# Kernel optimization log

Hardware: AMD Instinct MI355X
Metric: run time of the kernel (lower is better)

The kernel has to match this reference:

```python
import jax, jax.numpy as jnp
import numpy as np

B, N, E, D, H, C, U = 512, 256, 1024, 256, 256, 8, 64
MARGIN_T, RISK_T, SCALE = 0.2, 0.6, 0.1
NEG = -1.0e9


def setup_inputs() -> dict:
    key = jax.random.key(0)
    ks = jax.random.split(key, 30)
    s = 0.02
    inp = dict(
        features=jax.random.normal(ks[0], (B, D), jnp.float32),
        centered_scores=jax.random.normal(ks[1], (B, N), jnp.float32),
        margin=jax.random.uniform(ks[2], (B,), jnp.float32),
        boundary_risk=jax.random.uniform(ks[3], (B,), jnp.float32),
        edge_sensitivity=jax.random.normal(ks[4], (B, E), jnp.float32),
        coords=jax.random.normal(ks[5], (B, N, C), jnp.float32),
        uncertainty=jax.random.uniform(ks[6], (B, U), jnp.float32),
        Wc1=jax.random.normal(ks[7], (D, H), jnp.float32) * s,
        bc1=jnp.zeros((H,), jnp.float32),
        Wc2=jax.random.normal(ks[8], (H, H), jnp.float32) * s,
        bc2=jnp.zeros((H,), jnp.float32),
        Wn1=jax.random.normal(ks[9], (H + C + 2, H), jnp.float32) * s,
        bn1=jnp.zeros((H,), jnp.float32),
        Wn2=jax.random.normal(ks[10], (H, 1), jnp.float32) * s,
        bn2=jnp.zeros((1,), jnp.float32),
        We1=jax.random.normal(ks[11], (H + C + 2, H), jnp.float32) * s,
        be1=jnp.zeros((H,), jnp.float32),
        We2=jax.random.normal(ks[12], (H, 1), jnp.float32) * s,
        be2=jnp.zeros((1,), jnp.float32),
        Wg=jax.random.normal(ks[13], (H, 1), jnp.float32) * s,
        bg=jnp.zeros((1,), jnp.float32),
        action_mask=jax.random.bernoulli(ks[14], 0.8, (B, N)),
        edge_mask=jax.random.bernoulli(ks[15], 0.8, (B, E)),
        actions=jax.random.randint(ks[16], (B, N), 0, U, jnp.int32),
        edges=jax.random.randint(ks[17], (B, E, 2), 0, N, jnp.int32),
    )
    return inp


def _mlp2(x, W1, b1, W2, b2):
    return jax.nn.relu(x @ W1 + b1) @ W2 + b2


def reference(features, centered_scores, margin, boundary_risk, edge_sensitivity,
              coords, uncertainty, Wc1, bc1, Wc2, bc2, Wn1, bn1, Wn2, bn2,
              We1, be1, We2, be2, Wg, bg, action_mask, edge_mask, actions, edges):
    amf = action_mask.astype(jnp.float32)
    emf = edge_mask.astype(jnp.float32)

    # context MLP
    h = jax.nn.relu(jax.nn.relu(features @ Wc1 + bc1) @ Wc2 + bc2)  # [B,H]

    low_margin = (margin < MARGIN_T).astype(jnp.float32)
    high_risk = (boundary_risk > RISK_T).astype(jnp.float32)
    learned_gate = jax.nn.sigmoid((h @ Wg + bg)[:, 0])
    refine_gate = jnp.maximum(jnp.maximum(low_margin, high_risk),
                              (learned_gate > 0.5).astype(jnp.float32))  # [B]

    # node features: [B,N,H+C+2]
    act = jnp.clip(actions, 0, U - 1)
    unc_g = jnp.take_along_axis(uncertainty, act, axis=1)  # [B,N]
    h_n = jnp.broadcast_to(h[:, None, :], (B, N, H))
    node_feats = jnp.concatenate(
        [h_n, coords, centered_scores[..., None], unc_g[..., None]], axis=-1)
    node_delta = _mlp2(node_feats, Wn1, bn1, Wn2, bn2)[..., 0] * amf  # [B,N]

    # edge features: gather src/dst coords
    e = jnp.clip(edges, 0, N - 1)
    src_c = jnp.take_along_axis(coords, e[:, :, 0:1], axis=1)  # [B,E,C]
    dst_c = jnp.take_along_axis(coords, e[:, :, 1:2], axis=1)  # [B,E,C]
    h_e = jnp.broadcast_to(h[:, None, :], (B, E, H))
    edge_feats = jnp.concatenate(
        [h_e, dst_c - src_c, edge_sensitivity[..., None], emf[..., None]], axis=-1)
    edge_delta = _mlp2(edge_feats, We1, be1, We2, be2)[..., 0] * emf  # [B,E]

    gate_node = refine_gate[:, None]
    refined_scores = (centered_scores + gate_node * SCALE * node_delta) * amf
    denom = jnp.clip(amf.sum(-1, keepdims=True), 1.0, None)  # [B,1]
    refined_scores = (refined_scores - refined_scores.sum(-1, keepdims=True) / denom) * amf

    refined_edge = (edge_sensitivity + gate_node * SCALE * edge_delta) * emf

    masked_top = jnp.where(action_mask, refined_scores, NEG)
    top_vals, top_idx = jax.lax.top_k(masked_top, 2)
    refined_margin = top_vals[:, 0] - top_vals[:, 1]

    # masked per-batch variance of refined_edge (biased), 0 if <=1 valid entry
    cnt = emf.sum(-1)
    cnt_c = jnp.clip(cnt, 1.0, None)
    mean = (refined_edge * emf).sum(-1) / cnt_c
    var = (emf * (refined_edge - mean[:, None]) ** 2).sum(-1) / cnt_c
    edge_var = jnp.where(cnt > 1.0, var, 0.0)

    unc_term = (unc_g * amf).sum(-1) / denom[:, 0]
    refined_risk = jnp.clip(
        jax.nn.sigmoid(-refined_margin) + 0.2 * edge_var + 0.1 * unc_term, 0.0, 1.0)

    return (refined_scores, refined_margin, refined_edge,
            top_idx[:, 0], refined_risk, refine_gate)
```

## Files before the change

kernel.cpp:

```cpp
#include <hip/hip_runtime.h>
#include <math.h>

#define B 512
#define N 256
#define E 1024
#define D 256
#define H 256
#define C 8
#define U 64

typedef __fp16 h2 __attribute__((ext_vector_type(2)));
union UF { float f; h2 h; unsigned u; };

__device__ __forceinline__ float bc_f(h2 h) { UF u; u.h = h; return u.f; }
__device__ __forceinline__ h2 bc_h(float f) { UF u; u.f = f; return u.h; }

#if __has_builtin(__builtin_amdgcn_cvt_pkrtz)
__device__ __forceinline__ h2 pkh(float a, float b) { return __builtin_amdgcn_cvt_pkrtz(a, b); }
#else
__device__ __forceinline__ h2 pkh(float a, float b) { h2 r; r.x = (__fp16)a; r.y = (__fp16)b; return r; }
#endif

#if __has_builtin(__builtin_amdgcn_fdot2)
__device__ __forceinline__ float FDOT2(h2 a, h2 b, float c) { return __builtin_amdgcn_fdot2(a, b, c, false); }
#else
__device__ __forceinline__ float FDOT2(h2 a, h2 b, float c) {
    return fmaf((float)a.x, (float)b.x, fmaf((float)a.y, (float)b.y, c));
}
#endif

__device__ __forceinline__ float mask_val(const void* m, long i, int flag) {
    if (flag == 1) return ((const unsigned char*)m)[i] ? 1.f : 0.f;
    if (flag == 2) return (((const float*)m)[i] != 0.f) ? 1.f : 0.f;
    return ((const int*)m)[i] ? 1.f : 0.f;
}

__device__ __forceinline__ float block_sum(float v, float* red) {
    int t = threadIdx.x;
    red[t] = v; __syncthreads();
    for (int s = 128; s > 0; s >>= 1) {
        if (t < s) red[t] += red[t + s];
        __syncthreads();
    }
    float r = red[0]; __syncthreads();
    return r;
}

__global__ __launch_bounds__(512) void k_h(
    const float* __restrict__ feat,
    const float* __restrict__ Wc1, const float* __restrict__ bc1,
    const float* __restrict__ Wc2, const float* __restrict__ bc2,
    const float* __restrict__ Wn1, const float* __restrict__ bn1,
    const float* __restrict__ We1, const float* __restrict__ be1,
    const float* __restrict__ Wg,  const float* __restrict__ bg,
    const float* __restrict__ margin, const float* __restrict__ brisk,
    const unsigned int* __restrict__ amask_words,
    float* __restrict__ base_n, float* __restrict__ base_e,
    float* __restrict__ out_gate, int* __restrict__ flag)
{
    __shared__ __align__(16) float sF[4][256];
    __shared__ __align__(16) float sH[4][256];
    __shared__ float red[512];
    __shared__ int cls0, cls1;

    int t = threadIdx.x;
    int w = t >> 8;
    int c = t & 255;
    int b0 = blockIdx.x * 4;
    int r0 = 2 * w, r1 = 2 * w + 1;

    if (blockIdx.x == 0) {
        if (t == 0) { cls0 = 0; cls1 = 0; }
        __syncthreads();
        if (t < 256) {
            unsigned int wd = amask_words[t];
            if (wd != 0u && wd != 1u) {
                if (wd == 0x3f800000u) atomicOr(&cls1, 1);
                else                   atomicOr(&cls0, 1);
            }
        }
        __syncthreads();
        if (t == 0) *flag = cls0 ? 1 : (cls1 ? 2 : 0);
    }

    sF[r0][c] = feat[(long)(b0 + r0) * D + c];
    sF[r1][c] = feat[(long)(b0 + r1) * D + c];
    __syncthreads();

    {
        float aA[2] = {bc1[c], 0.f}, aB[2] = {bc1[c], 0.f};
        const float* Wp = Wc1 + c;
        for (int d0 = 0; d0 < D; d0 += 16) {
            float wv[16];
            #pragma unroll
            for (int k = 0; k < 16; k++) wv[k] = Wp[(long)(d0 + k) * H];
            #pragma unroll
            for (int k = 0; k < 16; k++) {
                aA[k & 1] = fmaf(sF[r0][d0 + k], wv[k], aA[k & 1]);
                aB[k & 1] = fmaf(sF[r1][d0 + k], wv[k], aB[k & 1]);
            }
        }
        sH[r0][c] = fmaxf(aA[0] + aA[1], 0.f);
        sH[r1][c] = fmaxf(aB[0] + aB[1], 0.f);
    }
    __syncthreads();

    {
        float aA[2] = {bc2[c], 0.f}, aB[2] = {bc2[c], 0.f};
        const float* Wp = Wc2 + c;
        for (int d0 = 0; d0 < H; d0 += 16) {
            float wv[16];
            #pragma unroll
            for (int k = 0; k < 16; k++) wv[k] = Wp[(long)(d0 + k) * H];
            #pragma unroll
            for (int k = 0; k < 16; k++) {
                aA[k & 1] = fmaf(sH[r0][d0 + k], wv[k], aA[k & 1]);
                aB[k & 1] = fmaf(sH[r1][d0 + k], wv[k], aB[k & 1]);
            }
        }
        float hA = fmaxf(aA[0] + aA[1], 0.f);
        float hB = fmaxf(aB[0] + aB[1], 0.f);
        __syncthreads();
        sF[r0][c] = hA;
        sF[r1][c] = hB;
    }
    __syncthreads();

    #pragma unroll
    for (int rr = 0; rr < 2; rr++) {
        int r = 2 * w + rr;
        red[t] = sF[r][c] * Wg[c];
        __syncthreads();
        for (int s = 128; s > 0; s >>= 1) {
            if (c < s) red[t] += red[t + s];
            __syncthreads();
        }
        if (c == 0) {
            int b = b0 + r;
            float lg = 1.f / (1.f + expf(-(red[t] + bg[0])));
            out_gate[b] = ((margin[b] < 0.2f) || (brisk[b] > 0.6f) || (lg > 0.5f)) ? 1.f : 0.f;
        }
        __syncthreads();
    }

    {
        const float* W3  = w ? (We1 + c) : (Wn1 + c);
        float bias       = w ? be1[c]    : bn1[c];
        float* dst       = w ? base_e    : base_n;
        float aA[2] = {bias, 0.f}, aB[2] = {bias, 0.f};
        float aC[2] = {bias, 0.f}, aD[2] = {bias, 0.f};
        for (int d0 = 0; d0 < H; d0 += 16) {
            float wv[16];
            #pragma unroll
            for (int k = 0; k < 16; k++) wv[k] = W3[(long)(d0 + k) * H];
            #pragma unroll
            for (int k = 0; k < 16; k++) {
                aA[k & 1] = fmaf(sF[0][d0 + k], wv[k], aA[k & 1]);
                aB[k & 1] = fmaf(sF[1][d0 + k], wv[k], aB[k & 1]);
                aC[k & 1] = fmaf(sF[2][d0 + k], wv[k], aC[k & 1]);
                aD[k & 1] = fmaf(sF[3][d0 + k], wv[k], aD[k & 1]);
            }
        }
        dst[(long)(b0 + 0) * H + c] = aA[0] + aA[1];
        dst[(long)(b0 + 1) * H + c] = aB[0] + aB[1];
        dst[(long)(b0 + 2) * H + c] = aC[0] + aC[1];
        dst[(long)(b0 + 3) * H + c] = aD[0] + aD[1];
    }
}

__global__ __launch_bounds__(256, 2) void k_ne(
    const float* __restrict__ cs, const float* __restrict__ coords,
    const float* __restrict__ unc, const int* __restrict__ actions,
    const void* __restrict__ amask,
    const float* __restrict__ Wn1, const float* __restrict__ Wn2,
    const float* __restrict__ bn2, const float* __restrict__ base_n,
    const float* __restrict__ es, const int* __restrict__ edges,
    const void* __restrict__ emask,
    const float* __restrict__ We1, const float* __restrict__ We2,
    const float* __restrict__ be2, const float* __restrict__ base_e,
    const float* __restrict__ gate, const int* __restrict__ flagp,
    float* __restrict__ out0, float* __restrict__ out1,
    float* __restrict__ out2, float* __restrict__ out3,
    float* __restrict__ riskbase, float* __restrict__ evar)
{
    __shared__ __align__(16) float smem[4864];
    int t = threadIdx.x;
    int w = t >> 6, lane = t & 63;
    int flag = *flagp;

    if (blockIdx.x < 128) {
        float* pack = smem;
        float* sB   = smem + 3072;
        int b0 = blockIdx.x * 4;

        {
            float* p = pack + t * 12;
            #pragma unroll
            for (int k = 0; k < 10; k++) p[k] = Wn1[(long)(H + k) * H + t];
            p[10] = Wn2[t];
            p[11] = 0.f;
            #pragma unroll
            for (int r = 0; r < 4; r++)
                sB[r * 256 + t] = base_n[(long)(b0 + r) * H + t];
        }
        __syncthreads();

        int b = b0 + w;
        float g = gate[b];
        float b2v = bn2[0];

        float f8v[4], ug[4], amv[4], acc[4];
        float f0[4], f1[4], f2[4], f3[4], f4[4], f5[4], f6[4], f7[4];
        #pragma unroll
        for (int q = 0; q < 4; q++) {
            int n = q * 64 + lane;
            const float4* cp = (const float4*)(coords + ((long)b * N + n) * C);
            float4 c0 = cp[0], c1 = cp[1];
            f0[q] = c0.x; f1[q] = c0.y; f2[q] = c0.z; f3[q] = c0.w;
            f4[q] = c1.x; f5[q] = c1.y; f6[q] = c1.z; f7[q] = c1.w;
            f8v[q] = cs[(long)b * N + n];
            int a = actions[(long)b * N + n];
            a = min(max(a, 0), U - 1);
            ug[q] = unc[(long)b * U + a];
            amv[q] = mask_val(amask, (long)b * N + n, flag);
            acc[q] = b2v;
        }

        float raw[4];
        if (g != 0.f) {
            const float* sBw = sB + w * 256;
            #pragma unroll 4
            for (int j = 0; j < H; j++) {
                const float* pj = pack + j * 12;
                float4 wa = *(const float4*)(pj);
                float4 wb = *(const float4*)(pj + 4);
                float4 wc = *(const float4*)(pj + 8);
                float bse = sBw[j];
                #pragma unroll
                for (int q = 0; q < 4; q++) {
                    float zA = fmaf(f0[q], wa.x, bse);
                    zA = fmaf(f1[q], wa.y, zA);
                    zA = fmaf(f2[q], wa.z, zA);
                    zA = fmaf(f3[q], wa.w, zA);
                    float zB = f4[q] * wb.x;
                    zB = fmaf(f5[q], wb.y, zB);
                    zB = fmaf(f6[q], wb.z, zB);
                    zB = fmaf(f7[q], wb.w, zB);
                    zB = fmaf(f8v[q], wc.x, zB);
                    zB = fmaf(ug[q], wc.y, zB);
                    acc[q] = fmaf(fmaxf(zA + zB, 0.f), wc.z, acc[q]);
                }
            }
            #pragma unroll
            for (int q = 0; q < 4; q++)
                raw[q] = (f8v[q] + g * 0.1f * (acc[q] * amv[q])) * amv[q];
        } else {
            #pragma unroll
            for (int q = 0; q < 4; q++) raw[q] = f8v[q] * amv[q];
        }

        float s = 0.f, cn = 0.f, su = 0.f;
        #pragma unroll
        for (int q = 0; q < 4; q++) {
            s += raw[q]; cn += amv[q]; su += ug[q] * amv[q];
        }
        #pragma unroll
        for (int m = 1; m < 64; m <<= 1) {
            s  += __shfl_xor(s, m);
            cn += __shfl_xor(cn, m);
            su += __shfl_xor(su, m);
        }
        float denom = fmaxf(cn, 1.f);
        float mu = s / denom;

        float rs[4], masked[4];
        #pragma unroll
        for (int q = 0; q < 4; q++) {
            rs[q] = (raw[q] - mu) * amv[q];
            out0[(long)b * N + q * 64 + lane] = rs[q];
            masked[q] = (amv[q] != 0.f) ? rs[q] : -1e9f;
        }

        float v1 = masked[0]; int i1 = lane; float v2 = -1e9f;
        #pragma unroll
        for (int q = 1; q < 4; q++) {
            float mv = masked[q]; int mi = q * 64 + lane;
            if (mv > v1) { v2 = v1; v1 = mv; i1 = mi; }
            else v2 = fmaxf(v2, mv);
        }
        #pragma unroll
        for (int m = 1; m < 64; m <<= 1) {
            float ov1 = __shfl_xor(v1, m);
            int   oi1 = __shfl_xor(i1, m);
            float ov2 = __shfl_xor(v2, m);
            bool ow = (ov1 > v1) || (ov1 == v1 && oi1 < i1);
            float lv  = ow ? v1 : ov1;
            float wv2 = ow ? ov2 : v2;
            if (ow) { v1 = ov1; i1 = oi1; }
            v2 = fmaxf(lv, wv2);
        }

        if (lane == 0) {
            float rmargin = v1 - v2;
            out1[b] = rmargin;
            out3[b] = (float)i1;
            float sig = 1.f / (1.f + expf(rmargin));
            riskbase[b] = sig + 0.1f * (su / denom);
        }
    } else {
        float*  A4 = smem;
        float2* B2 = (float2*)(smem + 1024);
        float*  sC = smem + 1536;
        float*  red = smem + 4608;
        int b = blockIdx.x - 128;
        float g = gate[b];

        float re[4], emv[4];
        if (g != 0.f) {
            {
                const float4* g4 = (const float4*)(coords + (long)b * N * C);
                float4 c0 = g4[2 * t], c1 = g4[2 * t + 1];
                float4* d0 = (float4*)(sC + t * 12);
                d0[0] = c0; d0[1] = c1;

                float w0 = We1[(long)(H + 0) * H + t];
                float w1 = We1[(long)(H + 1) * H + t];
                float w2 = We1[(long)(H + 2) * H + t];
                float w3 = We1[(long)(H + 3) * H + t];
                float w4 = We1[(long)(H + 4) * H + t];
                float w5 = We1[(long)(H + 5) * H + t];
                float w6 = We1[(long)(H + 6) * H + t];
                float w7 = We1[(long)(H + 7) * H + t];
                float w8 = We1[(long)(H + 8) * H + t];
                float w9 = We1[(long)(H + 9) * H + t];
                float we2 = We2[t];
                float bse = base_e[(long)b * H + t] + w9;
                float4 av;
                av.x = bc_f(pkh(w0, w1)); av.y = bc_f(pkh(w2, w3));
                av.z = bc_f(pkh(w4, w5)); av.w = bc_f(pkh(w6, w7));
                ((float4*)A4)[t] = av;
                B2[t] = make_float2(bc_f(pkh(w8, we2)), bse);
            }
            float b2v = be2[0];
            __syncthreads();

            float p01[4], p23[4], p45[4], p67[4], pes[4], esv[4], acc[4];
            #pragma unroll
            for (int q = 0; q < 4; q++) {
                int e = w * 256 + q * 64 + lane;
                long idx = (long)b * E + e;
                int2 ev = ((const int2*)edges)[idx];
                int s0 = min(max(ev.x, 0), N - 1);
                int d0 = min(max(ev.y, 0), N - 1);
                const float4* cs4 = (const float4*)(sC + s0 * 12);
                const float4* cd4 = (const float4*)(sC + d0 * 12);
                float4 sa = cs4[0], sb = cs4[1];
                float4 da = cd4[0], db = cd4[1];
                p01[q] = bc_f(pkh(da.x - sa.x, da.y - sa.y));
                p23[q] = bc_f(pkh(da.z - sa.z, da.w - sa.w));
                p45[q] = bc_f(pkh(db.x - sb.x, db.y - sb.y));
                p67[q] = bc_f(pkh(db.z - sb.z, db.w - sb.w));
                esv[q] = es[idx];
                pes[q] = bc_f(pkh(esv[q], 0.f));
                emv[q] = mask_val(emask, idx, flag);
                acc[q] = b2v;
            }

            const float4* A4v = (const float4*)A4;
            #pragma unroll 2
            for (int j = 0; j < H; j++) {
                float4 av = A4v[j];
                float2 bv = B2[j];
                h2 w01 = bc_h(av.x), w23 = bc_h(av.y);
                h2 w45 = bc_h(av.z), w67 = bc_h(av.w);
                h2 w8x = bc_h(bv.x);
                float we2f = (float)(w8x.y);
                float bse = bv.y;
                #pragma unroll
                for (int q = 0; q < 4; q++) {
                    float z = FDOT2(bc_h(p01[q]), w01, bse);
                    z = FDOT2(bc_h(p23[q]), w23, z);
                    z = FDOT2(bc_h(p45[q]), w45, z);
                    z = FDOT2(bc_h(p67[q]), w67, z);
                    z = FDOT2(bc_h(pes[q]), w8x, z);
                    acc[q] = fmaf(fmaxf(z, 0.f), we2f, acc[q]);
                }
            }

            #pragma unroll
            for (int q = 0; q < 4; q++) {
                long idx = (long)b * E + w * 256 + q * 64 + lane;
                re[q] = (emv[q] != 0.f) ? (esv[q] + g * 0.1f * acc[q]) : 0.f;
                out2[idx] = re[q];
            }
            __syncthreads();
        } else {
            #pragma unroll
            for (int q = 0; q < 4; q++) {
                long idx = (long)b * E + w * 256 + q * 64 + lane;
                emv[q] = mask_val(emask, idx, flag);
                re[q] = es[idx] * emv[q];
                out2[idx] = re[q];
            }
        }

        float S1 = 0.f, ce = 0.f;
        #pragma unroll
        for (int q = 0; q < 4; q++) { S1 += re[q]; ce += emv[q]; }
        float S1t = block_sum(S1, red);
        float cet = block_sum(ce, red);
        float mean = S1t / fmaxf(cet, 1.f);
        float v = 0.f;
        #pragma unroll
        for (int q = 0; q < 4; q++) {
            float dd = re[q] - mean;
            v = fmaf(emv[q] * dd, dd, v);
        }
        float vt = block_sum(v, red);
        if (t == 0) {
            float var = vt / fmaxf(cet, 1.f);
            evar[b] = (cet > 1.f) ? var : 0.f;
        }
    }
}

__global__ __launch_bounds__(256) void k_risk(
    const float* __restrict__ riskbase, const float* __restrict__ evar,
    float* __restrict__ out4)
{
    int b = blockIdx.x * 256 + threadIdx.x;
    float r = riskbase[b] + 0.2f * evar[b];
    out4[b] = fminf(fmaxf(r, 0.f), 1.f);
}

extern "C" void kernel_launch(void* const* d_in, const int* in_sizes, int n_in,
                              void* d_out, int out_size, void* d_ws, size_t ws_size,
                              hipStream_t stream) {
    const float* feat   = (const float*)d_in[0];
    const float* cs     = (const float*)d_in[1];
    const float* marg   = (const float*)d_in[2];
    const float* brisk  = (const float*)d_in[3];
    const float* es     = (const float*)d_in[4];
    const float* coords = (const float*)d_in[5];
    const float* unc    = (const float*)d_in[6];
    const float* Wc1    = (const float*)d_in[7];
    const float* bc1    = (const float*)d_in[8];
    const float* Wc2    = (const float*)d_in[9];
    const float* bc2    = (const float*)d_in[10];
    const float* Wn1    = (const float*)d_in[11];
    const float* bn1    = (const float*)d_in[12];
    const float* Wn2    = (const float*)d_in[13];
    const float* bn2    = (const float*)d_in[14];
    const float* We1    = (const float*)d_in[15];
    const float* be1    = (const float*)d_in[16];
    const float* We2    = (const float*)d_in[17];
    const float* be2    = (const float*)d_in[18];
    const float* Wg     = (const float*)d_in[19];
    const float* bg     = (const float*)d_in[20];
    const void*  amask  = d_in[21];
    const void*  emask  = d_in[22];
    const int*   actions= (const int*)d_in[23];
    const int*   edges  = (const int*)d_in[24];

    float* out0 = (float*)d_out;
    float* out1 = out0 + (long)B * N;
    float* out2 = out1 + B;
    float* out3 = out2 + (long)B * E;
    float* out4 = out3 + B;
    float* out5 = out4 + B;

    float* base_n   = (float*)d_ws;
    float* base_e   = base_n + (long)B * H;
    float* riskbase = base_e + (long)B * H;
    float* evar     = riskbase + B;
    int*   flag     = (int*)(evar + B);

    k_h<<<B / 4, 512, 0, stream>>>(feat, Wc1, bc1, Wc2, bc2, Wn1, bn1, We1, be1,
                                   Wg, bg, marg, brisk,
                                   (const unsigned int*)amask,
                                   base_n, base_e, out5, flag);
    k_ne<<<128 + B, 256, 0, stream>>>(cs, coords, unc, actions, amask,
                                      Wn1, Wn2, bn2, base_n,
                                      es, edges, emask,
                                      We1, We2, be2, base_e,
                                      out5, flag,
                                      out0, out1, out2, out3, riskbase, evar);
    k_risk<<<2, 256, 0, stream>>>(riskbase, evar, out4);
}
```

Baseline: 82.29 us.

## Split hidden dimension across two blocks with atomic accumulation and separate finalize kernel

Splits the node and edge MLP hidden-unit loop (H=256) into two halves handled by separate blocks. Partial sums are accumulated into zero-initialized buffers (node_delta, out2) with atomicAdd. Masking, centering, top-2, variance and risk computation move into a new k_fin kernel. This doubles the block count of the heavy kernel to improve parallelism and occupancy. In exchange it adds an extra kernel launch, zeroing writes, atomic traffic and a global round trip for the partial sums, and float atomics make summation order nondeterministic.

```diff
diff --git a/kernel.cpp b/kernel.cpp
--- a/kernel.cpp
+++ b/kernel.cpp
@@ -56,7 +56,8 @@
     const float* __restrict__ margin, const float* __restrict__ brisk,
     const unsigned int* __restrict__ amask_words,
     float* __restrict__ base_n, float* __restrict__ base_e,
-    float* __restrict__ out_gate, int* __restrict__ flag)
+    float* __restrict__ out_gate, int* __restrict__ flag,
+    float* __restrict__ node_delta, float* __restrict__ out2)
 {
     __shared__ __align__(16) float sF[4][256];
     __shared__ __align__(16) float sH[4][256];
@@ -68,6 +69,15 @@
     int c = t & 255;
     int b0 = blockIdx.x * 4;
     int r0 = 2 * w, r1 = 2 * w + 1;
+
+    {
+        int idx = blockIdx.x * 512 + t;
+        node_delta[idx] = 0.f;
+        node_delta[idx + 65536] = 0.f;
+        float4 z4 = make_float4(0.f, 0.f, 0.f, 0.f);
+        ((float4*)out2)[idx] = z4;
+        ((float4*)out2)[idx + 65536] = z4;
+    }
 
     if (blockIdx.x == 0) {
         if (t == 0) { cls0 = 0; cls1 = 0; }
@@ -171,66 +181,62 @@
 __global__ __launch_bounds__(256, 2) void k_ne(
     const float* __restrict__ cs, const float* __restrict__ coords,
     const float* __restrict__ unc, const int* __restrict__ actions,
-    const void* __restrict__ amask,
     const float* __restrict__ Wn1, const float* __restrict__ Wn2,
-    const float* __restrict__ bn2, const float* __restrict__ base_n,
+    const float* __restrict__ base_n,
     const float* __restrict__ es, const int* __restrict__ edges,
-    const void* __restrict__ emask,
     const float* __restrict__ We1, const float* __restrict__ We2,
-    const float* __restrict__ be2, const float* __restrict__ base_e,
-    const float* __restrict__ gate, const int* __restrict__ flagp,
-    float* __restrict__ out0, float* __restrict__ out1,
-    float* __restrict__ out2, float* __restrict__ out3,
-    float* __restrict__ riskbase, float* __restrict__ evar)
+    const float* __restrict__ base_e,
+    const float* __restrict__ gate,
+    float* __restrict__ node_delta, float* __restrict__ out2)
 {
-    __shared__ __align__(16) float smem[4864];
+    __shared__ __align__(16) float smem[4096];
     int t = threadIdx.x;
     int w = t >> 6, lane = t & 63;
-    int flag = *flagp;
-
-    if (blockIdx.x < 128) {
+
+    if (blockIdx.x < 256) {
+        int rg = blockIdx.x >> 1;
+        int jh = blockIdx.x & 1;
+        int b0 = rg * 4;
         float* pack = smem;
-        float* sB   = smem + 3072;
-        int b0 = blockIdx.x * 4;
-
+        float* sB   = smem + 1536;
+
+        if (t < 128) {
+            float* p = pack + t * 12;
+            int j = jh * 128 + t;
+            #pragma unroll
+            for (int k = 0; k < 10; k++) p[k] = Wn1[(long)(H + k) * H + j];
+            p[10] = Wn2[j];
+            p[11] = 0.f;
+        }
         {
-            float* p = pack + t * 12;
-            #pragma unroll
-            for (int k = 0; k < 10; k++) p[k] = Wn1[(long)(H + k) * H + t];
-            p[10] = Wn2[t];
-            p[11] = 0.f;
-            #pragma unroll
-            for (int r = 0; r < 4; r++)
-                sB[r * 256 + t] = base_n[(long)(b0 + r) * H + t];
+            int r = t >> 7, c0 = t & 127;
+            sB[r * 128 + c0]       = base_n[(long)(b0 + r) * H + jh * 128 + c0];
+            sB[(r + 2) * 128 + c0] = base_n[(long)(b0 + r + 2) * H + jh * 128 + c0];
         }
         __syncthreads();
 
         int b = b0 + w;
         float g = gate[b];
-        float b2v = bn2[0];
-
-        float f8v[4], ug[4], amv[4], acc[4];
-        float f0[4], f1[4], f2[4], f3[4], f4[4], f5[4], f6[4], f7[4];
-        #pragma unroll
-        for (int q = 0; q < 4; q++) {
-            int n = q * 64 + lane;
-            const float4* cp = (const float4*)(coords + ((long)b * N + n) * C);
-            float4 c0 = cp[0], c1 = cp[1];
-            f0[q] = c0.x; f1[q] = c0.y; f2[q] = c0.z; f3[q] = c0.w;
-            f4[q] = c1.x; f5[q] = c1.y; f6[q] = c1.z; f7[q] = c1.w;
-            f8v[q] = cs[(long)b * N + n];
-            int a = actions[(long)b * N + n];
-            a = min(max(a, 0), U - 1);
-            ug[q] = unc[(long)b * U + a];
-            amv[q] = mask_val(amask, (long)b * N + n, flag);
-            acc[q] = b2v;
-        }
-
-        float raw[4];
         if (g != 0.f) {
-            const float* sBw = sB + w * 256;
+            float f8v[4], ug[4], acc[4];
+            float f0[4], f1[4], f2[4], f3[4], f4[4], f5[4], f6[4], f7[4];
+            #pragma unroll
+            for (int q = 0; q < 4; q++) {
+                int n = q * 64 + lane;
+                const float4* cp = (const float4*)(coords + ((long)b * N + n) * C);
+                float4 c0 = cp[0], c1 = cp[1];
+                f0[q] = c0.x; f1[q] = c0.y; f2[q] = c0.z; f3[q] = c0.w;
+                f4[q] = c1.x; f5[q] = c1.y; f6[q] = c1.z; f7[q] = c1.w;
+                f8v[q] = cs[(long)b * N + n];
+                int a = actions[(long)b * N + n];
+                a = min(max(a, 0), U - 1);
+                ug[q] = unc[(long)b * U + a];
+                acc[q] = 0.f;
+            }
+
+            const float* sBw = sB + w * 128;
             #pragma unroll 4
-            for (int j = 0; j < H; j++) {
+            for (int j = 0; j < 128; j++) {
                 const float* pj = pack + j * 12;
                 float4 wa = *(const float4*)(pj);
                 float4 wb = *(const float4*)(pj + 4);
@@ -251,157 +257,171 @@
                     acc[q] = fmaf(fmaxf(zA + zB, 0.f), wc.z, acc[q]);
                 }
             }
+
             #pragma unroll
             for (int q = 0; q < 4; q++)
-                raw[q] = (f8v[q] + g * 0.1f * (acc[q] * amv[q])) * amv[q];
-        } else {
-            #pragma unroll
-            for (int q = 0; q < 4; q++) raw[q] = f8v[q] * amv[q];
-        }
-
-        float s = 0.f, cn = 0.f, su = 0.f;
+                atomicAdd(&node_delta[(long)b * N + q * 64 + lane], acc[q]);
+        }
+    } else {
+        int eb = blockIdx.x - 256;
+        int b = eb >> 1, jh = eb & 1;
+        float g = gate[b];
+        if (g == 0.f) return;
+
+        float*  A4 = smem;
+        float2* B2 = (float2*)(smem + 512);
+        float*  sC = smem + 1024;
+
+        {
+            const float4* g4 = (const float4*)(coords + (long)b * N * C);
+            float4 c0 = g4[2 * t], c1 = g4[2 * t + 1];
+            float4* d0 = (float4*)(sC + t * 12);
+            d0[0] = c0; d0[1] = c1;
+        }
+        if (t < 128) {
+            int j = jh * 128 + t;
+            float w0 = We1[(long)(H + 0) * H + j];
+            float w1 = We1[(long)(H + 1) * H + j];
+            float w2 = We1[(long)(H + 2) * H + j];
+            float w3 = We1[(long)(H + 3) * H + j];
+            float w4 = We1[(long)(H + 4) * H + j];
+            float w5 = We1[(long)(H + 5) * H + j];
+            float w6 = We1[(long)(H + 6) * H + j];
+            float w7 = We1[(long)(H + 7) * H + j];
+            float w8 = We1[(long)(H + 8) * H + j];
+            float w9 = We1[(long)(H + 9) * H + j];
+            float we2 = We2[j];
+            float bse = base_e[(long)b * H + j] + w9;
+            float4 av;
+            av.x = bc_f(pkh(w0, w1)); av.y = bc_f(pkh(w2, w3));
+            av.z = bc_f(pkh(w4, w5)); av.w = bc_f(pkh(w6, w7));
+            ((float4*)A4)[t] = av;
+            B2[t] = make_float2(bc_f(pkh(w8, we2)), bse);
+        }
+        __syncthreads();
+
+        float p01[4], p23[4], p45[4], p67[4], pes[4], acc[4];
         #pragma unroll
         for (int q = 0; q < 4; q++) {
-            s += raw[q]; cn += amv[q]; su += ug[q] * amv[q];
-        }
+            int e = w * 256 + q * 64 + lane;
+            long idx = (long)b * E + e;
+            int2 ev = ((const int2*)edges)[idx];
+            int s0 = min(max(ev.x, 0), N - 1);
+            int d0 = min(max(ev.y, 0), N - 1);
+            const float4* cs4 = (const float4*)(sC + s0 * 12);
+            const float4* cd4 = (const float4*)(sC + d0 * 12);
+            float4 sa = cs4[0], sb = cs4[1];
+            float4 da = cd4[0], db = cd4[1];
+            p01[q] = bc_f(pkh(da.x - sa.x, da.y - sa.y));
+            p23[q] = bc_f(pkh(da.z - sa.z, da.w - sa.w));
+            p45[q] = bc_f(pkh(db.x - sb.x, db.y - sb.y));
+            p67[q] = bc_f(pkh(db.z - sb.z, db.w - sb.w));
+            pes[q] = bc_f(pkh(es[idx], 0.f));
+            acc[q] = 0.f;
+        }
+
+        const float4* A4v = (const float4*)A4;
+        #pragma unroll 4
+        for (int j = 0; j < 128; j++) {
+            float4 av = A4v[j];
+            float2 bv = B2[j];
+            h2 w01 = bc_h(av.x), w23 = bc_h(av.y);
+            h2 w45 = bc_h(av.z), w67 = bc_h(av.w);
+            h2 w8x = bc_h(bv.x);
+            float we2f = (float)(w8x.y);
+            float bse = bv.y;
+            #pragma unroll
+            for (int q = 0; q < 4; q++) {
+                float z = FDOT2(bc_h(p01[q]), w01, bse);
+                z = FDOT2(bc_h(p23[q]), w23, z);
+                z = FDOT2(bc_h(p45[q]), w45, z);
+                z = FDOT2(bc_h(p67[q]), w67, z);
+                z = FDOT2(bc_h(pes[q]), w8x, z);
+                acc[q] = fmaf(fmaxf(z, 0.f), we2f, acc[q]);
+            }
+        }
+
         #pragma unroll
-        for (int m = 1; m < 64; m <<= 1) {
-            s  += __shfl_xor(s, m);
-            cn += __shfl_xor(cn, m);
-            su += __shfl_xor(su, m);
-        }
-        float denom = fmaxf(cn, 1.f);
-        float mu = s / denom;
-
-        float rs[4], masked[4];
-        #pragma unroll
-        for (int q = 0; q < 4; q++) {
-            rs[q] = (raw[q] - mu) * amv[q];
-            out0[(long)b * N + q * 64 + lane] = rs[q];
-            masked[q] = (amv[q] != 0.f) ? rs[q] : -1e9f;
-        }
-
-        float v1 = masked[0]; int i1 = lane; float v2 = -1e9f;
-        #pragma unroll
-        for (int q = 1; q < 4; q++) {
-            float mv = masked[q]; int mi = q * 64 + lane;
-            if (mv > v1) { v2 = v1; v1 = mv; i1 = mi; }
-            else v2 = fmaxf(v2, mv);
-        }
-        #pragma unroll
-        for (int m = 1; m < 64; m <<= 1) {
-            float ov1 = __shfl_xor(v1, m);
-            int   oi1 = __shfl_xor(i1, m);
-            float ov2 = __shfl_xor(v2, m);
-            bool ow = (ov1 > v1) || (ov1 == v1 && oi1 < i1);
-            float lv  = ow ? v1 : ov1;
-            float wv2 = ow ? ov2 : v2;
-            if (ow) { v1 = ov1; i1 = oi1; }
-            v2 = fmaxf(lv, wv2);
-        }
-
-        if (lane == 0) {
-            float rmargin = v1 - v2;
+        for (int q = 0; q < 4; q++)
+            atomicAdd(&out2[(long)b * E + w * 256 + q * 64 + lane], acc[q]);
+    }
+}
+
+__global__ __launch_bounds__(256) void k_fin(
+    const void* __restrict__ amask, const void* __restrict__ emask,
+    const int* __restrict__ actions, const float* __restrict__ unc,
+    const float* __restrict__ cs, const float* __restrict__ es,
+    const float* __restrict__ bn2, const float* __restrict__ be2,
+    const float* __restrict__ gate, const int* __restrict__ flagp,
+    const float* __restrict__ node_delta,
+    float* __restrict__ out0, float* __restrict__ out1,
+    float* __restrict__ out2, float* __restrict__ out3,
+    float* __restrict__ riskbase, float* __restrict__ evar)
+{
+    __shared__ float red[256];
+    __shared__ int ridx[256];
+    int t = threadIdx.x;
+    int flag = *flagp;
+
+    if (blockIdx.x < B) {
+        int b = blockIdx.x;
+        float g = gate[b];
+        float am = mask_val(amask, (long)b * N + t, flag);
+        float csv = cs[(long)b * N + t];
+        int a = actions[(long)b * N + t];
+        a = min(max(a, 0), U - 1);
+        float ug = unc[(long)b * U + a];
+        float nd = (node_delta[(long)b * N + t] + bn2[0]) * am;
+        float raw = (csv + g * 0.1f * nd) * am;
+
+        float sum = block_sum(raw, red);
+        float cnt = block_sum(am, red);
+        float denom = fmaxf(cnt, 1.f);
+        float rs = (raw - sum / denom) * am;
+        out0[(long)b * N + t] = rs;
+
+        float masked = (am != 0.f) ? rs : -1e9f;
+
+        red[t] = masked; ridx[t] = t; __syncthreads();
+        for (int s = 128; s > 0; s >>= 1) {
+            if (t < s) {
+                float o = red[t + s]; int oi = ridx[t + s];
+                if (o > red[t] || (o == red[t] && oi < ridx[t])) { red[t] = o; ridx[t] = oi; }
+            }
+            __syncthreads();
+        }
+        float v1 = red[0]; int i1 = ridx[0]; __syncthreads();
+
+        red[t] = (t == i1) ? -1e9f : masked; __syncthreads();
+        for (int s = 128; s > 0; s >>= 1) {
+            if (t < s) red[t] = fmaxf(red[t], red[t + s]);
+            __syncthreads();
+        }
+        float v2 = red[0]; __syncthreads();
+        float rmargin = v1 - v2;
+
+        float su = block_sum(ug * am, red);
+
+        if (t == 0) {
             out1[b] = rmargin;
             out3[b] = (float)i1;
             float sig = 1.f / (1.f + expf(rmargin));
             riskbase[b] = sig + 0.1f * (su / denom);
         }
     } else {
-        float*  A4 = smem;
-        float2* B2 = (float2*)(smem + 1024);
-        float*  sC = smem + 1536;
-        float*  red = smem + 4608;
-        int b = blockIdx.x - 128;
+        int b = blockIdx.x - B;
         float g = gate[b];
+        float be2v = be2[0];
 
         float re[4], emv[4];
-        if (g != 0.f) {
-            {
-                const float4* g4 = (const float4*)(coords + (long)b * N * C);
-                float4 c0 = g4[2 * t], c1 = g4[2 * t + 1];
-                float4* d0 = (float4*)(sC + t * 12);
-                d0[0] = c0; d0[1] = c1;
-
-                float w0 = We1[(long)(H + 0) * H + t];
-                float w1 = We1[(long)(H + 1) * H + t];
-                float w2 = We1[(long)(H + 2) * H + t];
-                float w3 = We1[(long)(H + 3) * H + t];
-                float w4 = We1[(long)(H + 4) * H + t];
-                float w5 = We1[(long)(H + 5) * H + t];
-                float w6 = We1[(long)(H + 6) * H + t];
-                float w7 = We1[(long)(H + 7) * H + t];
-                float w8 = We1[(long)(H + 8) * H + t];
-                float w9 = We1[(long)(H + 9) * H + t];
-                float we2 = We2[t];
-                float bse = base_e[(long)b * H + t] + w9;
-                float4 av;
-                av.x = bc_f(pkh(w0, w1)); av.y = bc_f(pkh(w2, w3));
-                av.z = bc_f(pkh(w4, w5)); av.w = bc_f(pkh(w6, w7));
-                ((float4*)A4)[t] = av;
-                B2[t] = make_float2(bc_f(pkh(w8, we2)), bse);
-            }
-            float b2v = be2[0];
-            __syncthreads();
-
-            float p01[4], p23[4], p45[4], p67[4], pes[4], esv[4], acc[4];
-            #pragma unroll
-            for (int q = 0; q < 4; q++) {
-                int e = w * 256 + q * 64 + lane;
-                long idx = (long)b * E + e;
-                int2 ev = ((const int2*)edges)[idx];
-                int s0 = min(max(ev.x, 0), N - 1);
-                int d0 = min(max(ev.y, 0), N - 1);
-                const float4* cs4 = (const float4*)(sC + s0 * 12);
-                const float4* cd4 = (const float4*)(sC + d0 * 12);
-                float4 sa = cs4[0], sb = cs4[1];
-                float4 da = cd4[0], db = cd4[1];
-                p01[q] = bc_f(pkh(da.x - sa.x, da.y - sa.y));
-                p23[q] = bc_f(pkh(da.z - sa.z, da.w - sa.w));
-                p45[q] = bc_f(pkh(db.x - sb.x, db.y - sb.y));
-                p67[q] = bc_f(pkh(db.z - sb.z, db.w - sb.w));
-                esv[q] = es[idx];
-                pes[q] = bc_f(pkh(esv[q], 0.f));
-                emv[q] = mask_val(emask, idx, flag);
-                acc[q] = b2v;
-            }
-
-            const float4* A4v = (const float4*)A4;
-            #pragma unroll 2
-            for (int j = 0; j < H; j++) {
-                float4 av = A4v[j];
-                float2 bv = B2[j];
-                h2 w01 = bc_h(av.x), w23 = bc_h(av.y);
-                h2 w45 = bc_h(av.z), w67 = bc_h(av.w);
-                h2 w8x = bc_h(bv.x);
-                float we2f = (float)(w8x.y);
-                float bse = bv.y;
-                #pragma unroll
-                for (int q = 0; q < 4; q++) {
-                    float z = FDOT2(bc_h(p01[q]), w01, bse);
-                    z = FDOT2(bc_h(p23[q]), w23, z);
-                    z = FDOT2(bc_h(p45[q]), w45, z);
-                    z = FDOT2(bc_h(p67[q]), w67, z);
-                    z = FDOT2(bc_h(pes[q]), w8x, z);
-                    acc[q] = fmaf(fmaxf(z, 0.f), we2f, acc[q]);
-                }
-            }
-
-            #pragma unroll
-            for (int q = 0; q < 4; q++) {
-                long idx = (long)b * E + w * 256 + q * 64 + lane;
-                re[q] = (emv[q] != 0.f) ? (esv[q] + g * 0.1f * acc[q]) : 0.f;
-                out2[idx] = re[q];
-            }
-            __syncthreads();
-        } else {
-            #pragma unroll
-            for (int q = 0; q < 4; q++) {
-                long idx = (long)b * E + w * 256 + q * 64 + lane;
-                emv[q] = mask_val(emask, idx, flag);
-                re[q] = es[idx] * emv[q];
-                out2[idx] = re[q];
-            }
+        #pragma unroll
+        for (int q = 0; q < 4; q++) {
+            long idx = (long)b * E + t + 256 * q;
+            emv[q] = mask_val(emask, idx, flag);
+            float delta = out2[idx] + be2v;
+            float r = es[idx] + g * 0.1f * delta;
+            re[q] = (emv[q] != 0.f) ? r : 0.f;
+            out2[idx] = re[q];
         }
 
         float S1 = 0.f, ce = 0.f;
@@ -469,21 +489,25 @@
     float* out4 = out3 + B;
     float* out5 = out4 + B;
 
-    float* base_n   = (float*)d_ws;
-    float* base_e   = base_n + (long)B * H;
-    float* riskbase = base_e + (long)B * H;
-    float* evar     = riskbase + B;
-    int*   flag     = (int*)(evar + B);
+    float* base_n     = (float*)d_ws;
+    float* base_e     = base_n + (long)B * H;
+    float* node_delta = base_e + (long)B * H;
+    float* riskbase   = node_delta + (long)B * N;
+    float* evar       = riskbase + B;
+    int*   flag       = (int*)(evar + B);
 
     k_h<<<B / 4, 512, 0, stream>>>(feat, Wc1, bc1, Wc2, bc2, Wn1, bn1, We1, be1,
                                    Wg, bg, marg, brisk,
                                    (const unsigned int*)amask,
-                                   base_n, base_e, out5, flag);
-    k_ne<<<128 + B, 256, 0, stream>>>(cs, coords, unc, actions, amask,
-                                      Wn1, Wn2, bn2, base_n,
-                                      es, edges, emask,
-                                      We1, We2, be2, base_e,
-                                      out5, flag,
-                                      out0, out1, out2, out3, riskbase, evar);
+                                   base_n, base_e, out5, flag,
+                                   node_delta, out2);
+    k_ne<<<256 + 2 * B, 256, 0, stream>>>(cs, coords, unc, actions,
+                                          Wn1, Wn2, base_n,
+                                          es, edges,
+                                          We1, We2, base_e,
+                                          out5, node_delta, out2);
+    k_fin<<<2 * B, 256, 0, stream>>>(amask, emask, actions, unc, cs, es,
+                                     bn2, be2, out5, flag, node_delta,
+                                     out0, out1, out2, out3, riskbase, evar);
     k_risk<<<2, 256, 0, stream>>>(riskbase, evar, out4);
 }
```

New measurement: 77.54 us. 1.06x faster.

## Split hidden-dim reduction across two waves per row in node/edge kernel

Applied to the files above, without the earlier changes.

Doubles the k_ne block to 512 threads. Each pair of waves splits the 256-wide hidden loop into two halves, and the partial sums are combined through shared memory. Weight packing and coordinate/base loads are spread across the two thread halves, and the variance reduction now runs over 512 threads. The aim is more parallelism per block to hide latency in the per-node and per-edge MLP loop. In exchange it costs extra syncs, shared-memory traffic, and idle half-waves during the epilogue. k_risk is also collapsed to a single block.

```diff
diff --git a/kernel.cpp b/kernel.cpp
--- a/kernel.cpp
+++ b/kernel.cpp
@@ -35,10 +35,10 @@
     return ((const int*)m)[i] ? 1.f : 0.f;
 }
 
-__device__ __forceinline__ float block_sum(float v, float* red) {
+__device__ __forceinline__ float block_sum512(float v, float* red) {
     int t = threadIdx.x;
     red[t] = v; __syncthreads();
-    for (int s = 128; s > 0; s >>= 1) {
+    for (int s = 256; s > 0; s >>= 1) {
         if (t < s) red[t] += red[t + s];
         __syncthreads();
     }
@@ -168,7 +168,7 @@
     }
 }
 
-__global__ __launch_bounds__(256, 2) void k_ne(
+__global__ __launch_bounds__(512) void k_ne(
     const float* __restrict__ cs, const float* __restrict__ coords,
     const float* __restrict__ unc, const int* __restrict__ actions,
     const void* __restrict__ amask,
@@ -183,7 +183,7 @@
     float* __restrict__ out2, float* __restrict__ out3,
     float* __restrict__ riskbase, float* __restrict__ evar)
 {
-    __shared__ __align__(16) float smem[4864];
+    __shared__ __align__(16) float smem[6144];
     int t = threadIdx.x;
     int w = t >> 6, lane = t & 63;
     int flag = *flagp;
@@ -191,25 +191,28 @@
     if (blockIdx.x < 128) {
         float* pack = smem;
         float* sB   = smem + 3072;
+        float* sAcc = smem + 4096;
         int b0 = blockIdx.x * 4;
 
-        {
+        if (t < 256) {
             float* p = pack + t * 12;
             #pragma unroll
             for (int k = 0; k < 10; k++) p[k] = Wn1[(long)(H + k) * H + t];
             p[10] = Wn2[t];
             p[11] = 0.f;
+        } else {
+            int i = t - 256;
             #pragma unroll
             for (int r = 0; r < 4; r++)
-                sB[r * 256 + t] = base_n[(long)(b0 + r) * H + t];
-        }
-        __syncthreads();
-
-        int b = b0 + w;
+                sB[r * 256 + i] = base_n[(long)(b0 + r) * H + i];
+        }
+        __syncthreads();
+
+        int r = w >> 1, jh = w & 1;
+        int b = b0 + r;
         float g = gate[b];
-        float b2v = bn2[0];
-
-        float f8v[4], ug[4], amv[4], acc[4];
+
+        float f8v[4], ug[4], acc[4];
         float f0[4], f1[4], f2[4], f3[4], f4[4], f5[4], f6[4], f7[4];
         #pragma unroll
         for (int q = 0; q < 4; q++) {
@@ -222,15 +225,15 @@
             int a = actions[(long)b * N + n];
             a = min(max(a, 0), U - 1);
             ug[q] = unc[(long)b * U + a];
-            amv[q] = mask_val(amask, (long)b * N + n, flag);
-            acc[q] = b2v;
-        }
-
-        float raw[4];
+            acc[q] = 0.f;
+        }
+
         if (g != 0.f) {
-            const float* sBw = sB + w * 256;
+            const float* sBw = sB + r * 256;
+            int jbase = jh * 128;
             #pragma unroll 4
-            for (int j = 0; j < H; j++) {
+            for (int jj = 0; jj < 128; jj++) {
+                int j = jbase + jj;
                 const float* pj = pack + j * 12;
                 float4 wa = *(const float4*)(pj);
                 float4 wb = *(const float4*)(pj + 4);
@@ -251,12 +254,23 @@
                     acc[q] = fmaf(fmaxf(zA + zB, 0.f), wc.z, acc[q]);
                 }
             }
-            #pragma unroll
-            for (int q = 0; q < 4; q++)
-                raw[q] = (f8v[q] + g * 0.1f * (acc[q] * amv[q])) * amv[q];
-        } else {
-            #pragma unroll
-            for (int q = 0; q < 4; q++) raw[q] = f8v[q] * amv[q];
+        }
+
+        if (jh == 1) {
+            #pragma unroll
+            for (int q = 0; q < 4; q++) sAcc[r * 256 + q * 64 + lane] = acc[q];
+        }
+        __syncthreads();
+        if (jh != 0) return;
+
+        float b2v = bn2[0];
+        float amv[4], raw[4];
+        #pragma unroll
+        for (int q = 0; q < 4; q++) {
+            acc[q] += sAcc[r * 256 + q * 64 + lane];
+            amv[q] = mask_val(amask, (long)b * N + q * 64 + lane, flag);
+            float nd = (acc[q] + b2v) * amv[q];
+            raw[q] = (f8v[q] + g * 0.1f * nd) * amv[q];
         }
 
         float s = 0.f, cn = 0.f, su = 0.f;
@@ -308,46 +322,48 @@
             riskbase[b] = sig + 0.1f * (su / denom);
         }
     } else {
-        float*  A4 = smem;
-        float2* B2 = (float2*)(smem + 1024);
-        float*  sC = smem + 1536;
-        float*  red = smem + 4608;
+        float*  A4  = smem;
+        float2* B2  = (float2*)(smem + 1024);
+        float*  sC  = smem + 1536;
+        float*  sAcc= smem + 4608;
+        float*  red = smem + 5632;
         int b = blockIdx.x - 128;
         float g = gate[b];
+        int iq = w >> 1, jh = w & 1;
 
         float re[4], emv[4];
         if (g != 0.f) {
-            {
-                const float4* g4 = (const float4*)(coords + (long)b * N * C);
-                float4 c0 = g4[2 * t], c1 = g4[2 * t + 1];
-                float4* d0 = (float4*)(sC + t * 12);
-                d0[0] = c0; d0[1] = c1;
-
-                float w0 = We1[(long)(H + 0) * H + t];
-                float w1 = We1[(long)(H + 1) * H + t];
-                float w2 = We1[(long)(H + 2) * H + t];
-                float w3 = We1[(long)(H + 3) * H + t];
-                float w4 = We1[(long)(H + 4) * H + t];
-                float w5 = We1[(long)(H + 5) * H + t];
-                float w6 = We1[(long)(H + 6) * H + t];
-                float w7 = We1[(long)(H + 7) * H + t];
-                float w8 = We1[(long)(H + 8) * H + t];
-                float w9 = We1[(long)(H + 9) * H + t];
-                float we2 = We2[t];
-                float bse = base_e[(long)b * H + t] + w9;
+            if (t < 256) {
+                int j = t;
+                float w0 = We1[(long)(H + 0) * H + j];
+                float w1 = We1[(long)(H + 1) * H + j];
+                float w2 = We1[(long)(H + 2) * H + j];
+                float w3 = We1[(long)(H + 3) * H + j];
+                float w4 = We1[(long)(H + 4) * H + j];
+                float w5 = We1[(long)(H + 5) * H + j];
+                float w6 = We1[(long)(H + 6) * H + j];
+                float w7 = We1[(long)(H + 7) * H + j];
+                float w8 = We1[(long)(H + 8) * H + j];
+                float w9 = We1[(long)(H + 9) * H + j];
+                float we2 = We2[j];
+                float bse = base_e[(long)b * H + j] + w9;
                 float4 av;
                 av.x = bc_f(pkh(w0, w1)); av.y = bc_f(pkh(w2, w3));
                 av.z = bc_f(pkh(w4, w5)); av.w = bc_f(pkh(w6, w7));
-                ((float4*)A4)[t] = av;
-                B2[t] = make_float2(bc_f(pkh(w8, we2)), bse);
-            }
-            float b2v = be2[0];
+                ((float4*)A4)[j] = av;
+                B2[j] = make_float2(bc_f(pkh(w8, we2)), bse);
+            } else {
+                int n = t - 256;
+                const float4* g4 = (const float4*)(coords + ((long)b * N + n) * C);
+                float4* d0 = (float4*)(sC + n * 12);
+                d0[0] = g4[0]; d0[1] = g4[1];
+            }
             __syncthreads();
 
             float p01[4], p23[4], p45[4], p67[4], pes[4], esv[4], acc[4];
             #pragma unroll
             for (int q = 0; q < 4; q++) {
-                int e = w * 256 + q * 64 + lane;
+                int e = iq * 256 + q * 64 + lane;
                 long idx = (long)b * E + e;
                 int2 ev = ((const int2*)edges)[idx];
                 int s0 = min(max(ev.x, 0), N - 1);
@@ -362,13 +378,14 @@
                 p67[q] = bc_f(pkh(db.z - sb.z, db.w - sb.w));
                 esv[q] = es[idx];
                 pes[q] = bc_f(pkh(esv[q], 0.f));
-                emv[q] = mask_val(emask, idx, flag);
-                acc[q] = b2v;
+                acc[q] = 0.f;
             }
 
             const float4* A4v = (const float4*)A4;
-            #pragma unroll 2
-            for (int j = 0; j < H; j++) {
+            int jbase = jh * 128;
+            #pragma unroll 4
+            for (int jj = 0; jj < 128; jj++) {
+                int j = jbase + jj;
                 float4 av = A4v[j];
                 float2 bv = B2[j];
                 h2 w01 = bc_h(av.x), w23 = bc_h(av.y);
@@ -387,28 +404,49 @@
                 }
             }
 
-            #pragma unroll
-            for (int q = 0; q < 4; q++) {
-                long idx = (long)b * E + w * 256 + q * 64 + lane;
-                re[q] = (emv[q] != 0.f) ? (esv[q] + g * 0.1f * acc[q]) : 0.f;
-                out2[idx] = re[q];
+            if (jh == 1) {
+                #pragma unroll
+                for (int q = 0; q < 4; q++)
+                    sAcc[iq * 256 + q * 64 + lane] = acc[q];
             }
             __syncthreads();
+
+            float be2v = be2[0];
+            if (jh == 0) {
+                #pragma unroll
+                for (int q = 0; q < 4; q++) {
+                    int e = iq * 256 + q * 64 + lane;
+                    long idx = (long)b * E + e;
+                    acc[q] += sAcc[e];
+                    emv[q] = mask_val(emask, idx, flag);
+                    re[q] = (emv[q] != 0.f)
+                          ? (esv[q] + g * 0.1f * (acc[q] + be2v)) : 0.f;
+                    out2[idx] = re[q];
+                }
+            } else {
+                #pragma unroll
+                for (int q = 0; q < 4; q++) { re[q] = 0.f; emv[q] = 0.f; }
+            }
         } else {
-            #pragma unroll
-            for (int q = 0; q < 4; q++) {
-                long idx = (long)b * E + w * 256 + q * 64 + lane;
-                emv[q] = mask_val(emask, idx, flag);
-                re[q] = es[idx] * emv[q];
-                out2[idx] = re[q];
+            if (jh == 0) {
+                #pragma unroll
+                for (int q = 0; q < 4; q++) {
+                    long idx = (long)b * E + iq * 256 + q * 64 + lane;
+                    emv[q] = mask_val(emask, idx, flag);
+                    re[q] = es[idx] * emv[q];
+                    out2[idx] = re[q];
+                }
+            } else {
+                #pragma unroll
+                for (int q = 0; q < 4; q++) { re[q] = 0.f; emv[q] = 0.f; }
             }
         }
 
         float S1 = 0.f, ce = 0.f;
         #pragma unroll
         for (int q = 0; q < 4; q++) { S1 += re[q]; ce += emv[q]; }
-        float S1t = block_sum(S1, red);
-        float cet = block_sum(ce, red);
+        float S1t = block_sum512(S1, red);
+        float cet = block_sum512(ce, red);
         float mean = S1t / fmaxf(cet, 1.f);
         float v = 0.f;
         #pragma unroll
@@ -416,7 +454,7 @@
             float dd = re[q] - mean;
             v = fmaf(emv[q] * dd, dd, v);
         }
-        float vt = block_sum(v, red);
+        float vt = block_sum512(v, red);
         if (t == 0) {
             float var = vt / fmaxf(cet, 1.f);
             evar[b] = (cet > 1.f) ? var : 0.f;
@@ -424,11 +462,11 @@
     }
 }
 
-__global__ __launch_bounds__(256) void k_risk(
+__global__ __launch_bounds__(512) void k_risk(
     const float* __restrict__ riskbase, const float* __restrict__ evar,
     float* __restrict__ out4)
 {
-    int b = blockIdx.x * 256 + threadIdx.x;
+    int b = threadIdx.x + blockIdx.x * 512;
     float r = riskbase[b] + 0.2f * evar[b];
     out4[b] = fminf(fmaxf(r, 0.f), 1.f);
 }
@@ -479,11 +517,11 @@
                                    Wg, bg, marg, brisk,
                                    (const unsigned int*)amask,
                                    base_n, base_e, out5, flag);
-    k_ne<<<128 + B, 256, 0, stream>>>(cs, coords, unc, actions, amask,
+    k_ne<<<128 + B, 512, 0, stream>>>(cs, coords, unc, actions, amask,
                                       Wn1, Wn2, bn2, base_n,
                                       es, edges, emask,
                                       We1, We2, be2, base_e,
                                       out5, flag,
                                       out0, out1, out2, out3, riskbase, evar);
-    k_risk<<<2, 256, 0, stream>>>(riskbase, evar, out4);
-}
+    k_risk<<<1, 512, 0, stream>>>(riskbase, evar, out4);
+}
```

New measurement: 77.87 us. -5.4%, faster.
